# Kernel tuning notes

Hardware: AMD Instinct MI355X
Metric: run time of the kernel (lower is better)

The kernel has to match this reference:

```python
import jax, jax.numpy as jnp
import numpy as np

K = 7          # kernel_size
PAD = 3        # padding
GROUPS = 8
OUTC = 128
INC = 128
REFINE = True


def conv1x1(x, w):
    # x: [B,C,H,W], w: [O,C] (1x1 conv, no bias)
    return jnp.einsum('oc,bchw->bohw', w, x)


def unfold2d(x, k):
    # x: [B,C,Hp,Wp] -> [B,C,h,w,k,k], stride 1 (matches torch unfold(2,k).unfold(3,k))
    B, C, Hp, Wp = x.shape
    h, w = Hp - k + 1, Wp - k + 1
    patches = jnp.stack([x[:, :, i:i + h, j:j + w] for i in range(k) for j in range(k)], axis=-1)
    return patches.reshape(B, C, h, w, k, k)


def unfold1d(x, k, axis):
    # sliding window of size k, stride 1, along axis 2 (rows) or 3 (cols)
    if axis == 2:
        h = x.shape[2] - k + 1
        return jnp.stack([x[:, :, i:i + h, :] for i in range(k)], axis=-1)  # [B,C,h,W,k]
    else:
        w = x.shape[3] - k + 1
        return jnp.stack([x[:, :, :, j:j + w] for j in range(k)], axis=-1)  # [B,C,H,w,k]


def _forward(feature_map, wq, wk, wv, rel_h, rel_w):
    c = feature_map.shape[1] // 2
    fm_t0, fm_t1 = feature_map[:, :c], feature_map[:, c:]
    B, _, H, W = fm_t0.shape
    cg = OUTC // GROUPS

    padded_t0 = jnp.pad(fm_t0, ((0, 0), (0, 0), (PAD, PAD), (PAD, PAD)))
    q = conv1x1(fm_t1, wq)                 # [B,OUTC,H,W]
    k_full = conv1x1(padded_t0, wk)        # [B,OUTC,H+2p,W+2p]
    v_full = conv1x1(padded_t0, wv)

    k_win = unfold2d(k_full, K)            # [B,OUTC,H,W,K,K]
    k_h, k_w = k_win[:, :OUTC // 2], k_win[:, OUTC // 2:]
    k_win = jnp.concatenate([k_h + rel_h, k_w + rel_w], axis=1)
    k_win = k_win.reshape(B, GROUPS, cg, H, W, K * K)
    v_win = unfold2d(v_full, K).reshape(B, GROUPS, cg, H, W, K * K)

    qg = q.reshape(B, GROUPS, cg, H, W, 1)
    attn = jax.nn.softmax(jnp.sum(qg * k_win, axis=2), axis=-1)  # [B,G,H,W,K*K]
    out = jnp.einsum('bnhwk,bnchwk->bnchw', attn, v_win).reshape(B, OUTC, H, W)

    if REFINE:
        win = 2 * K + 1
        p_col = jnp.pad(fm_t0, ((0, 0), (0, 0), (K, K), (0, 0)))
        p_row = jnp.pad(fm_t0, ((0, 0), (0, 0), (0, 0), (K, K)))
        k_col = unfold1d(conv1x1(p_col, wk), win, 2).reshape(B, GROUPS, cg, H, W, win)
        k_row = unfold1d(conv1x1(p_row, wk), win, 3).reshape(B, GROUPS, cg, H, W, win)
        v_col = unfold1d(conv1x1(p_col, wv), win, 2).reshape(B, GROUPS, cg, H, W, win)
        v_row = unfold1d(conv1x1(p_row, wv), win, 3).reshape(B, GROUPS, cg, H, W, win)

        a_row = jax.nn.softmax(jnp.sum(qg * k_row, axis=2), axis=-1)
        a_col = jax.nn.softmax(jnp.sum(qg * k_col, axis=2), axis=-1)
        out = out + jnp.einsum('bnhwk,bnchwk->bnchw', a_row, v_row).reshape(B, OUTC, H, W)
        out = out + jnp.einsum('bnhwk,bnchwk->bnchw', a_col, v_col).reshape(B, OUTC, H, W)
    return out


def setup_inputs() -> dict:
    key = jax.random.key(0)
    ks = jax.random.split(key, 6)
    B, H, W = 2, 64, 64
    feature_map = jax.random.normal(ks[0], (B, 2 * INC, H, W), dtype=jnp.float32)
    # kaiming_normal fan_out for 1x1 conv: std = sqrt(2 / outc)
    std = float(np.sqrt(2.0 / OUTC))
    wq = jax.random.normal(ks[1], (OUTC, INC), dtype=jnp.float32) * std
    wk = jax.random.normal(ks[2], (OUTC, INC), dtype=jnp.float32) * std
    wv = jax.random.normal(ks[3], (OUTC, INC), dtype=jnp.float32) * std
    rel_h = jax.random.normal(ks[4], (OUTC // 2, 1, 1, K, 1), dtype=jnp.float32)
    rel_w = jax.random.normal(ks[5], (OUTC // 2, 1, 1, 1, K), dtype=jnp.float32)
    return {"feature_map": feature_map, "wq": wq, "wk": wk, "wv": wv,
            "rel_h": rel_h, "rel_w": rel_w}


def reference(feature_map, wq, wk, wv, rel_h, rel_w):
    return _forward(feature_map, wq, wk, wv, rel_h, rel_w)
```

## Files before the change

### kernel.cpp

```cpp
#include <hip/hip_runtime.h>
#include <hip/hip_bf16.h>

__device__ __forceinline__ float bf2f(unsigned short u) {
    union { unsigned int i; float f; } v; v.i = ((unsigned int)u) << 16; return v.f;
}
__device__ __forceinline__ unsigned short f2bf(float f) {
    __hip_bfloat16 h = __float2bfloat16(f);
    return *reinterpret_cast<unsigned short*>(&h);
}


__global__ __launch_bounds__(256) void conv_kernel(
    const float* __restrict__ fm,
    const float* __restrict__ wq, const float* __restrict__ wk,
    const float* __restrict__ wv,
    float* __restrict__ Qout,
    unsigned short* __restrict__ K0,
    unsigned short* __restrict__ V0)
{
    const int sel = blockIdx.y;
    const float* W = (sel == 0) ? wq : ((sel == 1) ? wk : wv);
    const int c0 = (sel == 0) ? 128 : 0;

    __shared__ float w_s[64 * 132];
    __shared__ float x_s[64 * 68];

    const int tid = threadIdx.x;
    const int P0  = blockIdx.x * 64;
    const int b   = P0 >> 12;
    const int hw0 = P0 & 4095;

    float acc[8][4];
    #pragma unroll
    for (int i = 0; i < 8; ++i)
        #pragma unroll
        for (int j = 0; j < 4; ++j) acc[i][j] = 0.f;

    const int ocb = (tid >> 4) * 8;
    const int pxb = (tid & 15) * 4;

    for (int kh = 0; kh < 128; kh += 64) {
        {
            const int o    = tid >> 1;
            const int koff = (tid & 1) * 32;
            #pragma unroll
            for (int i = 0; i < 8; ++i) {
                float4 v = *(const float4*)(W + o * 128 + kh + koff + i * 4);
                w_s[(koff + i * 4 + 0) * 132 + o] = v.x;
                w_s[(koff + i * 4 + 1) * 132 + o] = v.y;
                w_s[(koff + i * 4 + 2) * 132 + o] = v.z;
                w_s[(koff + i * 4 + 3) * 132 + o] = v.w;
            }
        }
        {
            const int c  = tid >> 2;
            const int pc = (tid & 3) * 16;
            const float* src = fm + (((size_t)(b * 256 + c0 + kh + c)) << 12) + hw0 + pc;
            #pragma unroll
            for (int i = 0; i < 4; ++i)
                *(float4*)(&x_s[c * 68 + pc + i * 4]) = *(const float4*)(src + i * 4);
        }
        __syncthreads();
        #pragma unroll 8
        for (int k = 0; k < 64; ++k) {
            const float* kw = &w_s[k * 132 + ocb];
            float4 wa = *(const float4*)kw;
            float4 wb = *(const float4*)(kw + 4);
            float4 xv = *(const float4*)(&x_s[k * 68 + pxb]);
            const float wf[8] = {wa.x, wa.y, wa.z, wa.w, wb.x, wb.y, wb.z, wb.w};
            const float xf[4] = {xv.x, xv.y, xv.z, xv.w};
            #pragma unroll
            for (int i = 0; i < 8; ++i)
                #pragma unroll
                for (int j = 0; j < 4; ++j) acc[i][j] += wf[i] * xf[j];
        }
        __syncthreads();
    }

    const int g   = ocb >> 4;
    const int lci = ocb & 8;
    #pragma unroll
    for (int pj = 0; pj < 4; ++pj) {
        const int hw = hw0 + pxb + pj;
        const size_t base = ((((size_t)(b * 8 + g)) << 12) + hw) * 16 + lci;
        if (sel == 0) {
            *(float4*)(Qout + base)     = make_float4(acc[0][pj], acc[1][pj], acc[2][pj], acc[3][pj]);
            *(float4*)(Qout + base + 4) = make_float4(acc[4][pj], acc[5][pj], acc[6][pj], acc[7][pj]);
        } else {
            unsigned short tmp[8];
            #pragma unroll
            for (int i = 0; i < 8; ++i) tmp[i] = f2bf(acc[i][pj]);
            unsigned short* dst = ((sel == 1) ? K0 : V0) + base;
            *(uint4*)dst = *(const uint4*)tmp;
        }
    }
}

struct KV16 { uint4 a, b; };
__device__ __forceinline__ KV16 ld16(const unsigned short* p) {
    KV16 r; r.a = *(const uint4*)p; r.b = *(const uint4*)(p + 8); return r;
}
__device__ __forceinline__ float dotq(const float* q, const KV16& k) {
    const unsigned short* u = (const unsigned short*)&k;
    float s = 0.f;
    #pragma unroll
    for (int c = 0; c < 16; ++c) s += q[c] * bf2f(u[c]);
    return s;
}
__device__ __forceinline__ void axpyq(float* acc, float wgt, const KV16& v) {
    const unsigned short* u = (const unsigned short*)&v;
    #pragma unroll
    for (int c = 0; c < 16; ++c) acc[c] += wgt * bf2f(u[c]);
}

__global__ __launch_bounds__(256) void attn_kernel(
    const float* __restrict__ Q,
    const unsigned short* __restrict__ K0,
    const unsigned short* __restrict__ V0,
    const float* __restrict__ rel_h,
    const float* __restrict__ rel_w,
    float* __restrict__ out)
{
    const int tid  = threadIdx.x;
    const int w    = tid & 63;
    const int h    = blockIdx.x * 4 + (tid >> 6);
    const int g    = blockIdx.y;
    const int b    = blockIdx.z / 3;
    const int part = blockIdx.z % 3;

    const size_t slab = ((size_t)(b * 8 + g)) << 16;
    const float* qptr = Q + slab + (size_t)(h * 64 + w) * 16;

    float qr[16];
    #pragma unroll
    for (int ci = 0; ci < 16; ++ci) qr[ci] = qptr[ci];

    const unsigned short* Kp = K0 + slab;
    const unsigned short* Vp = V0 + slab;

    float acc[16];
    #pragma unroll
    for (int ci = 0; ci < 16; ++ci) acc[ci] = 0.f;

    if (part == 0) {
        float qrel[7];
        const float* rel = (g < 4) ? (rel_h + g * 112) : (rel_w + (g - 4) * 112);
        #pragma unroll
        for (int t = 0; t < 7; ++t) {
            float s = 0.f;
            #pragma unroll
            for (int ci = 0; ci < 16; ++ci) s += qr[ci] * rel[ci * 7 + t];
            qrel[t] = s;
        }
        float sc[49];
        float mx = -3.4e38f;
        #pragma unroll
        for (int i = 0; i < 7; ++i) {
            const int y = h + i - 3;
            #pragma unroll
            for (int j = 0; j < 7; ++j) {
                const int x = w + j - 3;
                float d = 0.f;
                if (y >= 0 && y < 64 && x >= 0 && x < 64)
                    d = dotq(qr, ld16(Kp + (size_t)(y * 64 + x) * 16));
                d += qrel[(g < 4) ? i : j];
                sc[i * 7 + j] = d;
                mx = fmaxf(mx, d);
            }
        }
        float den = 0.f;
        #pragma unroll
        for (int k = 0; k < 49; ++k) { sc[k] = __expf(sc[k] - mx); den += sc[k]; }
        const float inv = 1.f / den;
        #pragma unroll
        for (int i = 0; i < 7; ++i) {
            const int y = h + i - 3;
            #pragma unroll
            for (int j = 0; j < 7; ++j) {
                const int x = w + j - 3;
                if (y >= 0 && y < 64 && x >= 0 && x < 64)
                    axpyq(acc, sc[i * 7 + j] * inv, ld16(Vp + (size_t)(y * 64 + x) * 16));
            }
        }
    } else if (part == 1) {
        float sc[15];
        float mx = -3.4e38f;
        #pragma unroll
        for (int j = 0; j < 15; ++j) {
            const int x = w + j - 7;
            float d = 0.f;
            if (x >= 0 && x < 64)
                d = dotq(qr, ld16(Kp + (size_t)(h * 64 + x) * 16));
            sc[j] = d; mx = fmaxf(mx, d);
        }
        float den = 0.f;
        #pragma unroll
        for (int j = 0; j < 15; ++j) { sc[j] = __expf(sc[j] - mx); den += sc[j]; }
        const float inv = 1.f / den;
        #pragma unroll
        for (int j = 0; j < 15; ++j) {
            const int x = w + j - 7;
            if (x >= 0 && x < 64)
                axpyq(acc, sc[j] * inv, ld16(Vp + (size_t)(h * 64 + x) * 16));
        }
    } else {
        float sc[15];
        float mx = -3.4e38f;
        #pragma unroll
        for (int i = 0; i < 15; ++i) {
            const int y = h + i - 7;
            float d = 0.f;
            if (y >= 0 && y < 64)
                d = dotq(qr, ld16(Kp + (size_t)(y * 64 + w) * 16));
            sc[i] = d; mx = fmaxf(mx, d);
        }
        float den = 0.f;
        #pragma unroll
        for (int i = 0; i < 15; ++i) { sc[i] = __expf(sc[i] - mx); den += sc[i]; }
        const float inv = 1.f / den;
        #pragma unroll
        for (int i = 0; i < 15; ++i) {
            const int y = h + i - 7;
            if (y >= 0 && y < 64)
                axpyq(acc, sc[i] * inv, ld16(Vp + (size_t)(y * 64 + w) * 16));
        }
    }

    float* op = out + (((size_t)(b * 128 + g * 16)) << 12) + h * 64 + w;
    #pragma unroll
    for (int ci = 0; ci < 16; ++ci)
        atomicAdd(op + ((size_t)ci << 12), acc[ci]);
}

extern "C" void kernel_launch(void* const* d_in, const int* in_sizes, int n_in,
                              void* d_out, int out_size, void* d_ws, size_t ws_size,
                              hipStream_t stream) {
    (void)in_sizes; (void)n_in; (void)ws_size;
    const float* fm    = (const float*)d_in[0];
    const float* wq    = (const float*)d_in[1];
    const float* wk    = (const float*)d_in[2];
    const float* wv    = (const float*)d_in[3];
    const float* rel_h = (const float*)d_in[4];
    const float* rel_w = (const float*)d_in[5];

    float* Q = (float*)d_ws;
    unsigned short* K0 = (unsigned short*)(Q + 1048576);
    unsigned short* V0 = K0 + 1048576;

    hipMemsetAsync(d_out, 0, (size_t)out_size * sizeof(float), stream);
    conv_kernel<<<dim3(128, 3, 1), dim3(256), 0, stream>>>(
        fm, wq, wk, wv, Q, K0, V0);
    attn_kernel<<<dim3(16, 8, 6), dim3(256), 0, stream>>>(
        Q, K0, V0, rel_h, rel_w, (float*)d_out);
}
```

Measured before the change: 115.7 us.

## Split channels across 4 lanes and fuse three attention parts per pixel

```diff
diff --git a/kernel.cpp b/kernel.cpp
--- a/kernel.cpp
+++ b/kernel.cpp
@@ -96,21 +96,24 @@
     }
 }
 
-struct KV16 { uint4 a, b; };
-__device__ __forceinline__ KV16 ld16(const unsigned short* p) {
-    KV16 r; r.a = *(const uint4*)p; r.b = *(const uint4*)(p + 8); return r;
-}
-__device__ __forceinline__ float dotq(const float* q, const KV16& k) {
-    const unsigned short* u = (const unsigned short*)&k;
-    float s = 0.f;
-    #pragma unroll
-    for (int c = 0; c < 16; ++c) s += q[c] * bf2f(u[c]);
+__device__ __forceinline__ float dot4(const float* q, const unsigned short* p) {
+    uint2 u = *(const uint2*)p;
+    const unsigned short* s = (const unsigned short*)&u;
+    return q[0] * bf2f(s[0]) + q[1] * bf2f(s[1]) +
+           q[2] * bf2f(s[2]) + q[3] * bf2f(s[3]);
+}
+__device__ __forceinline__ float red4(float s) {
+    s += __shfl_xor(s, 1, 64);
+    s += __shfl_xor(s, 2, 64);
     return s;
 }
-__device__ __forceinline__ void axpyq(float* acc, float wgt, const KV16& v) {
-    const unsigned short* u = (const unsigned short*)&v;
-    #pragma unroll
-    for (int c = 0; c < 16; ++c) acc[c] += wgt * bf2f(u[c]);
+__device__ __forceinline__ void axpy4(float* acc, float wgt, const unsigned short* p) {
+    uint2 u = *(const uint2*)p;
+    const unsigned short* s = (const unsigned short*)&u;
+    acc[0] += wgt * bf2f(s[0]);
+    acc[1] += wgt * bf2f(s[1]);
+    acc[2] += wgt * bf2f(s[2]);
+    acc[3] += wgt * bf2f(s[3]);
 }
 
 __global__ __launch_bounds__(256) void attn_kernel(
@@ -121,121 +124,143 @@
     const float* __restrict__ rel_w,
     float* __restrict__ out)
 {
-    const int tid  = threadIdx.x;
-    const int w    = tid & 63;
-    const int h    = blockIdx.x * 4 + (tid >> 6);
-    const int g    = blockIdx.y;
-    const int b    = blockIdx.z / 3;
-    const int part = blockIdx.z % 3;
+    const int tid = threadIdx.x;
+    const int cq  = tid & 3;
+    const int w   = tid >> 2;
+    const int h   = blockIdx.x;
+    const int g   = blockIdx.y;
+    const int b   = blockIdx.z;
+    const int cq4 = cq * 4;
 
     const size_t slab = ((size_t)(b * 8 + g)) << 16;
-    const float* qptr = Q + slab + (size_t)(h * 64 + w) * 16;
-
-    float qr[16];
-    #pragma unroll
-    for (int ci = 0; ci < 16; ++ci) qr[ci] = qptr[ci];
+    const float* qptr = Q + slab + (size_t)(h * 64 + w) * 16 + cq4;
+
+    float qr[4];
+    #pragma unroll
+    for (int c = 0; c < 4; ++c) qr[c] = qptr[c];
 
     const unsigned short* Kp = K0 + slab;
     const unsigned short* Vp = V0 + slab;
 
-    float acc[16];
-    #pragma unroll
-    for (int ci = 0; ci < 16; ++ci) acc[ci] = 0.f;
-
-    if (part == 0) {
+    float accT[4];
+    #pragma unroll
+    for (int c = 0; c < 4; ++c) accT[c] = 0.f;
+
+    {
         float qrel[7];
         const float* rel = (g < 4) ? (rel_h + g * 112) : (rel_w + (g - 4) * 112);
         #pragma unroll
         for (int t = 0; t < 7; ++t) {
             float s = 0.f;
             #pragma unroll
-            for (int ci = 0; ci < 16; ++ci) s += qr[ci] * rel[ci * 7 + t];
-            qrel[t] = s;
-        }
-        float sc[49];
-        float mx = -3.4e38f;
+            for (int c = 0; c < 4; ++c) s += qr[c] * rel[(cq4 + c) * 7 + t];
+            qrel[t] = red4(s);
+        }
+        const bool bias_i = (g < 4);
+
+        float m = -3.0e38f, den = 0.f;
+        float acc[4] = {0.f, 0.f, 0.f, 0.f};
         #pragma unroll
         for (int i = 0; i < 7; ++i) {
             const int y = h + i - 3;
+            const bool yin = ((unsigned)y < 64u);
+            float s[7];
             #pragma unroll
             for (int j = 0; j < 7; ++j) {
                 const int x = w + j - 3;
                 float d = 0.f;
-                if (y >= 0 && y < 64 && x >= 0 && x < 64)
-                    d = dotq(qr, ld16(Kp + (size_t)(y * 64 + x) * 16));
-                d += qrel[(g < 4) ? i : j];
-                sc[i * 7 + j] = d;
-                mx = fmaxf(mx, d);
+                if (yin && (unsigned)x < 64u)
+                    d = dot4(qr, Kp + (((size_t)(y * 64 + x)) << 4) + cq4);
+                d = red4(d);
+                s[j] = d + (bias_i ? qrel[i] : qrel[j]);
             }
-        }
-        float den = 0.f;
-        #pragma unroll
-        for (int k = 0; k < 49; ++k) { sc[k] = __expf(sc[k] - mx); den += sc[k]; }
+            float rm = s[0];
+            #pragma unroll
+            for (int j = 1; j < 7; ++j) rm = fmaxf(rm, s[j]);
+            const float nm  = fmaxf(m, rm);
+            const float scl = __expf(m - nm);
+            den *= scl;
+            #pragma unroll
+            for (int c = 0; c < 4; ++c) acc[c] *= scl;
+            #pragma unroll
+            for (int j = 0; j < 7; ++j) {
+                const float e = __expf(s[j] - nm);
+                den += e;
+                const int x = w + j - 3;
+                if (yin && (unsigned)x < 64u)
+                    axpy4(acc, e, Vp + (((size_t)(y * 64 + x)) << 4) + cq4);
+            }
+            m = nm;
+        }
         const float inv = 1.f / den;
         #pragma unroll
-        for (int i = 0; i < 7; ++i) {
-            const int y = h + i - 3;
-            #pragma unroll
-            for (int j = 0; j < 7; ++j) {
-                const int x = w + j - 3;
-                if (y >= 0 && y < 64 && x >= 0 && x < 64)
-                    axpyq(acc, sc[i * 7 + j] * inv, ld16(Vp + (size_t)(y * 64 + x) * 16));
-            }
-        }
-    } else if (part == 1) {
+        for (int c = 0; c < 4; ++c) accT[c] += acc[c] * inv;
+    }
+
+    {
         float sc[15];
-        float mx = -3.4e38f;
+        float mx = -3.0e38f;
         #pragma unroll
         for (int j = 0; j < 15; ++j) {
             const int x = w + j - 7;
             float d = 0.f;
-            if (x >= 0 && x < 64)
-                d = dotq(qr, ld16(Kp + (size_t)(h * 64 + x) * 16));
-            sc[j] = d; mx = fmaxf(mx, d);
+            if ((unsigned)x < 64u)
+                d = dot4(qr, Kp + (((size_t)(h * 64 + x)) << 4) + cq4);
+            sc[j] = red4(d);
+            mx = fmaxf(mx, sc[j]);
         }
         float den = 0.f;
         #pragma unroll
         for (int j = 0; j < 15; ++j) { sc[j] = __expf(sc[j] - mx); den += sc[j]; }
         const float inv = 1.f / den;
+        float acc[4] = {0.f, 0.f, 0.f, 0.f};
         #pragma unroll
         for (int j = 0; j < 15; ++j) {
             const int x = w + j - 7;
-            if (x >= 0 && x < 64)
-                axpyq(acc, sc[j] * inv, ld16(Vp + (size_t)(h * 64 + x) * 16));
-        }
-    } else {
+            if ((unsigned)x < 64u)
+                axpy4(acc, sc[j], Vp + (((size_t)(h * 64 + x)) << 4) + cq4);
+        }
+        #pragma unroll
+        for (int c = 0; c < 4; ++c) accT[c] += acc[c] * inv;
+    }
+
+    {
         float sc[15];
-        float mx = -3.4e38f;
+        float mx = -3.0e38f;
         #pragma unroll
         for (int i = 0; i < 15; ++i) {
             const int y = h + i - 7;
             float d = 0.f;
-            if (y >= 0 && y < 64)
-                d = dotq(qr, ld16(Kp + (size_t)(y * 64 + w) * 16));
-            sc[i] = d; mx = fmaxf(mx, d);
+            if ((unsigned)y < 64u)
+                d = dot4(qr, Kp + (((size_t)(y * 64 + w)) << 4) + cq4);
+            sc[i] = red4(d);
+            mx = fmaxf(mx, sc[i]);
         }
         float den = 0.f;
         #pragma unroll
         for (int i = 0; i < 15; ++i) { sc[i] = __expf(sc[i] - mx); den += sc[i]; }
         const float inv = 1.f / den;
+        float acc[4] = {0.f, 0.f, 0.f, 0.f};
         #pragma unroll
         for (int i = 0; i < 15; ++i) {
             const int y = h + i - 7;
-            if (y >= 0 && y < 64)
-                axpyq(acc, sc[i] * inv, ld16(Vp + (size_t)(y * 64 + w) * 16));
-        }
-    }
-
-    float* op = out + (((size_t)(b * 128 + g * 16)) << 12) + h * 64 + w;
-    #pragma unroll
-    for (int ci = 0; ci < 16; ++ci)
-        atomicAdd(op + ((size_t)ci << 12), acc[ci]);
+            if ((unsigned)y < 64u)
+                axpy4(acc, sc[i], Vp + (((size_t)(y * 64 + w)) << 4) + cq4);
+        }
+        #pragma unroll
+        for (int c = 0; c < 4; ++c) accT[c] += acc[c] * inv;
+    }
+
+    float* op = out + (((size_t)(b * 128 + g * 16 + cq4)) << 12) + h * 64 + w;
+    #pragma unroll
+    for (int c = 0; c < 4; ++c)
+        op[(size_t)c << 12] = accT[c];
 }
 
 extern "C" void kernel_launch(void* const* d_in, const int* in_sizes, int n_in,
                               void* d_out, int out_size, void* d_ws, size_t ws_size,
                               hipStream_t stream) {
-    (void)in_sizes; (void)n_in; (void)ws_size;
+    (void)in_sizes; (void)n_in; (void)ws_size; (void)out_size;
     const float* fm    = (const float*)d_in[0];
     const float* wq    = (const float*)d_in[1];
     const float* wk    = (const float*)d_in[2];
@@ -247,9 +272,8 @@
     unsigned short* K0 = (unsigned short*)(Q + 1048576);
     unsigned short* V0 = K0 + 1048576;
 
-    hipMemsetAsync(d_out, 0, (size_t)out_size * sizeof(float), stream);
     conv_kernel<<<dim3(128, 3, 1), dim3(256), 0, stream>>>(
         fm, wq, wk, wv, Q, K0, V0);
-    attn_kernel<<<dim3(16, 8, 6), dim3(256), 0, stream>>>(
+    attn_kernel<<<dim3(64, 8, 2), dim3(256), 0, stream>>>(
         Q, K0, V0, rel_h, rel_w, (float*)d_out);
 }
```

New measurement: 147.1 us. 1.27x slower.
